# Kernel optimization log

Hardware: AMD Instinct MI355X
Metric: run time of the kernel (lower is better)

Reference implementation:

```python
import jax, jax.numpy as jnp
import numpy as np


def conv2d(x, w, b, pad=0):
    y = jax.lax.conv_general_dilated(x, w, (1, 1), [(pad, pad), (pad, pad)],
                                     dimension_numbers=('NCHW', 'OIHW', 'NCHW'))
    return y + b[None, :, None, None]


def leaky(x):
    return jnp.where(x >= 0, x, 0.1 * x)


def adaptive_pool3(x):
    # exact AdaptiveAvgPool2d((3,3)) when H,W divisible by 3
    B, C, H, W = x.shape
    return x.reshape(B, C, 3, H // 3, 3, W // 3).mean(axis=(3, 5))


def psf2otf(ker, H, W):
    # circularly shift PSF so its centre is at (0,0), then FFT (DWDN convention)
    B, C, kh, kw = ker.shape
    c = kh // 2 + 1
    psf = jnp.zeros((B, C, H, W), ker.dtype)
    psf = psf.at[:, :, :c, :c].set(ker[:, :, c - 1:, c - 1:])
    psf = psf.at[:, :, :c, -(c - 1):].set(ker[:, :, c - 1:, :c - 1])
    psf = psf.at[:, :, -(c - 1):, :c].set(ker[:, :, :c - 1, c - 1:])
    psf = psf.at[:, :, -(c - 1):, -(c - 1):].set(ker[:, :, :c - 1, :c - 1])
    return jnp.fft.fft2(psf)


def setup_inputs() -> dict:
    key = jax.random.key(0)
    ks = jax.random.split(key, 16)
    B, NF, C, H = 8, 64, 16, 246
    x = jax.random.normal(ks[0], (B, NF, H, H), jnp.float32)
    kernel = jax.random.uniform(ks[1], (B, 1, 21, 21), jnp.float32)
    kernel = kernel / kernel.sum(axis=(2, 3), keepdims=True)  # normalized blur PSF
    def w(k, shape):
        fan_in = shape[1] * shape[2] * shape[3]
        return jax.random.normal(k, shape, jnp.float32) / np.sqrt(fan_in)
    return {
        'x': x, 'kernel': kernel,
        'w_red': w(ks[2], (C, NF, 1, 1)), 'b_red': jnp.zeros((C,), jnp.float32),
        'w_g1': w(ks[3], (C, C, 3, 3)), 'b_g1': jnp.zeros((C,), jnp.float32),
        'w_g2': w(ks[4], (C, C, 3, 3)), 'b_g2': jnp.zeros((C,), jnp.float32),
        'w_g3': w(ks[5], (C, C, 3, 3)), 'b_g3': jnp.zeros((C,), jnp.float32),
        'w_g4': w(ks[6], (C, C, 1, 1)), 'b_g4': jnp.zeros((C,), jnp.float32),
        'w_exp': w(ks[7], (NF, C, 1, 1)), 'b_exp': jnp.zeros((NF,), jnp.float32),
    }


def reference(x, kernel, w_red, b_red, w_g1, b_g1, w_g2, b_g2, w_g3, b_g3,
              w_g4, b_g4, w_exp, b_exp):
    cls_feats = conv2d(x, w_red, b_red)                      # [B,C,H,W]
    h = leaky(conv2d(cls_feats, w_g1, b_g1))                 # valid 3x3 convs
    h = leaky(conv2d(h, w_g2, b_g2))
    h = conv2d(h, w_g3, b_g3)
    h = adaptive_pool3(h)                                    # [B,C,3,3]
    kernel_P = jnp.exp(conv2d(h, w_g4, b_g4))
    kernel_P = kernel_P - kernel_P.mean(axis=(2, 3), keepdims=True)

    ks_ = kernel.shape[-1]
    fp = jnp.pad(cls_feats, ((0, 0), (0, 0), (ks_, ks_), (ks_, ks_)), mode='edge')
    Hp, Wp = fp.shape[2], fp.shape[3]
    # batched Wiener deconvolution over all channels at once (replaces per-channel loop)
    Kf = psf2otf(kernel, Hp, Wp)                             # [B,1,Hp,Wp] complex
    Pf = psf2otf(kernel_P, Hp, Wp)                           # [B,C,Hp,Wp] complex
    denom = Kf.real ** 2 + Kf.imag ** 2 + Pf.real ** 2 + Pf.imag ** 2
    inv_ker = jnp.conj(Kf) / denom                           # conj(K)/(|K|^2+|P|^2)
    deblur = jnp.fft.ifft2(inv_ker * jnp.fft.fft2(fp)).real
    clear = deblur[:, :, ks_:-ks_, ks_:-ks_]
    return conv2d(clear, w_exp, b_exp)
```

## Files before the change

kernel.cpp:

```cpp
#include <hip/hip_runtime.h>
#include <hip/hip_bf16.h>

__device__ inline float2 cadd(float2 a, float2 b){ return make_float2(a.x+b.x, a.y+b.y); }
__device__ inline float2 csub(float2 a, float2 b){ return make_float2(a.x-b.x, a.y-b.y); }
__device__ inline float2 cmul(float2 a, float2 b){
    return make_float2(fmaf(a.x,b.x,-a.y*b.y), fmaf(a.x,b.y,a.y*b.x));
}

#define NPIX 60516
#define NFFT 288
#define NFFT2 82944
#define XW 152
#define SPLANE (NFFT*XW)

__device__ inline int lidx(int i, int c){ return i*8 + (i>>2) + c; }
#define LDSN 2376

template<bool INV>
__device__ inline void bf4(float2 a0, float2 a1, float2 a2, float2 a3,
                           float2& b0, float2& b1, float2& b2, float2& b3) {
    float2 t0=cadd(a0,a2), t1=csub(a0,a2), t2=cadd(a1,a3), t3=csub(a1,a3);
    b0=cadd(t0,t2); b2=csub(t0,t2);
    if (!INV) { b1=make_float2(t1.x+t3.y, t1.y-t3.x); b3=make_float2(t1.x-t3.y, t1.y+t3.x); }
    else      { b1=make_float2(t1.x-t3.y, t1.y+t3.x); b3=make_float2(t1.x+t3.y, t1.y-t3.x); }
}
template<bool INV>
__device__ inline void bf3(float2 a0, float2 a1, float2 a2,
                           float2& b0, float2& b1, float2& b2) {
    const float d = INV ? 0.8660254037844386f : -0.8660254037844386f;
    float2 tt=cadd(a1,a2), u=csub(a1,a2);
    b0=cadd(a0,tt);
    b1=make_float2(a0.x-0.5f*tt.x - d*u.y, a0.y-0.5f*tt.y + d*u.x);
    b2=make_float2(a0.x-0.5f*tt.x + d*u.y, a0.y-0.5f*tt.y - d*u.x);
}

template<bool INV>
__device__ inline void fft288_row(float2*& X, float2*& Y, int lane, const float2* __restrict__ tw) {
    auto TW = [&](int k) { float2 v = tw[k]; if (INV) v.y = -v.y; return v; };
    for (int p = lane; p < 72; p += 64) {
        float2 b0,b1,b2,b3;
        bf4<INV>(X[p], X[p+72], X[p+144], X[p+216], b0,b1,b2,b3);
        Y[4*p]=b0; Y[4*p+1]=cmul(b1,TW(p)); Y[4*p+2]=cmul(b2,TW(2*p)); Y[4*p+3]=cmul(b3,TW(3*p));
    }
    __syncthreads(); { float2* t=X; X=Y; Y=t; }
    for (int it = lane; it < 72; it += 64) {
        int p = it>>2, q = it&3, i0 = q+4*p;
        float2 b0,b1,b2,b3;
        bf4<INV>(X[i0], X[i0+72], X[i0+144], X[i0+216], b0,b1,b2,b3);
        int o = q+16*p;
        Y[o]=b0; Y[o+4]=cmul(b1,TW(4*p)); Y[o+8]=cmul(b2,TW(8*p)); Y[o+12]=cmul(b3,TW(12*p));
    }
    __syncthreads(); { float2* t=X; X=Y; Y=t; }
    for (int it = lane; it < 144; it += 64) {
        int p = it>>4, q = it&15, i0 = q+16*p;
        float2 a0=X[i0], a1=X[i0+144];
        int o = q+32*p;
        Y[o]=cadd(a0,a1); Y[o+16]=cmul(csub(a0,a1),TW(16*p));
    }
    __syncthreads(); { float2* t=X; X=Y; Y=t; }
    for (int it = lane; it < 96; it += 64) {
        int p = it>>5, q = it&31, i0 = q+32*p;
        float2 b0,b1,b2;
        bf3<INV>(X[i0], X[i0+96], X[i0+192], b0,b1,b2);
        int o = q+96*p;
        Y[o]=b0; Y[o+32]=cmul(b1,TW(32*p)); Y[o+64]=cmul(b2,TW(64*p));
    }
    __syncthreads(); { float2* t=X; X=Y; Y=t; }
    for (int q = lane; q < 96; q += 64) {
        float2 b0,b1,b2;
        bf3<INV>(X[q], X[q+96], X[q+192], b0,b1,b2);
        Y[q]=b0; Y[q+96]=b1; Y[q+192]=b2;
    }
    __syncthreads(); { float2* t=X; X=Y; Y=t; }
}

template<bool INV>
__device__ inline void fft288_s9(float2*& X, float2*& Y, int w, int c, const float2* __restrict__ tw) {
    auto TW = [&](int k) { float2 v = tw[k]; if (INV) v.y = -v.y; return v; };
    for (int p = w; p < 72; p += 32) {
        float2 b0,b1,b2,b3;
        bf4<INV>(X[lidx(p,c)], X[lidx(p+72,c)], X[lidx(p+144,c)], X[lidx(p+216,c)], b0,b1,b2,b3);
        Y[lidx(4*p,c)]=b0; Y[lidx(4*p+1,c)]=cmul(b1,TW(p));
        Y[lidx(4*p+2,c)]=cmul(b2,TW(2*p)); Y[lidx(4*p+3,c)]=cmul(b3,TW(3*p));
    }
    __syncthreads(); { float2* t=X; X=Y; Y=t; }
    for (int it = w; it < 72; it += 32) {
        int p = it>>2, q = it&3, i0 = q+4*p;
        float2 b0,b1,b2,b3;
        bf4<INV>(X[lidx(i0,c)], X[lidx(i0+72,c)], X[lidx(i0+144,c)], X[lidx(i0+216,c)], b0,b1,b2,b3);
        int o = q+16*p;
        Y[lidx(o,c)]=b0; Y[lidx(o+4,c)]=cmul(b1,TW(4*p));
        Y[lidx(o+8,c)]=cmul(b2,TW(8*p)); Y[lidx(o+12,c)]=cmul(b3,TW(12*p));
    }
    __syncthreads(); { float2* t=X; X=Y; Y=t; }
    for (int it = w; it < 144; it += 32) {
        int p = it>>4, q = it&15, i0 = q+16*p;
        float2 a0=X[lidx(i0,c)], a1=X[lidx(i0+144,c)];
        int o = q+32*p;
        Y[lidx(o,c)]=cadd(a0,a1); Y[lidx(o+16,c)]=cmul(csub(a0,a1),TW(16*p));
    }
    __syncthreads(); { float2* t=X; X=Y; Y=t; }
    for (int it = w; it < 96; it += 32) {
        int p = it>>5, q = it&31, i0 = q+32*p;
        float2 b0,b1,b2;
        bf3<INV>(X[lidx(i0,c)], X[lidx(i0+96,c)], X[lidx(i0+192,c)], b0,b1,b2);
        int o = q+96*p;
        Y[lidx(o,c)]=b0; Y[lidx(o+32,c)]=cmul(b1,TW(32*p)); Y[lidx(o+64,c)]=cmul(b2,TW(64*p));
    }
    __syncthreads(); { float2* t=X; X=Y; Y=t; }
    for (int q = w; q < 96; q += 32) {
        float2 b0,b1,b2;
        bf3<INV>(X[lidx(q,c)], X[lidx(q+96,c)], X[lidx(q+192,c)], b0,b1,b2);
        Y[lidx(q,c)]=b0; Y[lidx(q+96,c)]=b1; Y[lidx(q+192,c)]=b2;
    }
    __syncthreads(); { float2* t=X; X=Y; Y=t; }
}

__global__ void k_tw(float2* tw, float* pooled) {
    int t = threadIdx.x;
    if (t < NFFT) {
        double ang = -2.0 * 3.14159265358979323846 * (double)t / (double)NFFT;
        tw[t] = make_float2((float)cos(ang), (float)sin(ang));
    }
    for (int i = t; i < 1152; i += 320) pooled[i] = 0.f;
}

__global__ __launch_bounds__(256) void k_conv1x1_red(const float* __restrict__ x,
        const float* __restrict__ w, const float* __restrict__ bias, float* __restrict__ out) {
    int idx = blockIdx.x * 256 + threadIdx.x;
    if (idx >= 8 * NPIX) return;
    int b = idx / NPIX, p = idx % NPIX;
    const float* xb = x + (size_t)b * 64 * NPIX + p;
    float acc[16];
    #pragma unroll
    for (int co = 0; co < 16; co++) acc[co] = bias[co];
    for (int ci = 0; ci < 64; ci++) {
        float v = xb[(size_t)ci * NPIX];
        #pragma unroll
        for (int co = 0; co < 16; co++) acc[co] = fmaf(w[co*64+ci], v, acc[co]);
    }
    float* ob = out + (size_t)b * 16 * NPIX + p;
    #pragma unroll
    for (int co = 0; co < 16; co++) ob[(size_t)co*NPIX] = acc[co];
}

template<int HIN, bool LEAKY>
__global__ __launch_bounds__(256) void k_conv3x3(const float* __restrict__ in,
        const float* __restrict__ w, const float* __restrict__ bias, float* __restrict__ out) {
    const int HOUT = HIN - 2;
    const int GX = (HOUT + 3) / 4;
    int idx = blockIdx.x * 256 + threadIdx.x;
    if (idx >= 8 * HOUT * GX) return;
    int b  = idx / (HOUT * GX);
    int r  = idx % (HOUT * GX);
    int oy = r / GX;
    int ox0 = (r % GX) * 4;

    float acc[16][4];
    #pragma unroll
    for (int co = 0; co < 16; co++) {
        float bb = bias[co];
        #pragma unroll
        for (int px = 0; px < 4; px++) acc[co][px] = bb;
    }
    const float* ib = in + (size_t)b * 16 * HIN * HIN + (size_t)oy * HIN;
    for (int ci = 0; ci < 16; ci++) {
        const float* ic = ib + (size_t)ci * HIN * HIN;
        #pragma unroll
        for (int ky = 0; ky < 3; ky++) {
            float in6[6];
            #pragma unroll
            for (int j = 0; j < 6; j++) {
                int xx = ox0 + j;
                if (HOUT % 4 != 0) { if (xx > HIN - 1) xx = HIN - 1; }
                in6[j] = ic[ky * HIN + xx];
            }
            #pragma unroll
            for (int kx = 0; kx < 3; kx++) {
                #pragma unroll
                for (int co = 0; co < 16; co++) {
                    float wv = w[co*144 + ci*9 + ky*3 + kx];
                    #pragma unroll
                    for (int px = 0; px < 4; px++)
                        acc[co][px] = fmaf(wv, in6[px + kx], acc[co][px]);
                }
            }
        }
    }
    float* ob = out + (size_t)b * 16 * HOUT * HOUT + (size_t)oy * HOUT + ox0;
    #pragma unroll
    for (int co = 0; co < 16; co++) {
        #pragma unroll
        for (int px = 0; px < 4; px++) {
            if (HOUT % 4 == 0 || ox0 + px < HOUT) {
                float v = acc[co][px];
                if (LEAKY) v = (v >= 0.f) ? v : 0.1f * v;
                ob[(size_t)co * HOUT * HOUT + px] = v;
            }
        }
    }
}

__global__ __launch_bounds__(256) void k_conv3x3_pool(const float* __restrict__ in,
        const float* __restrict__ w, const float* __restrict__ bias, float* __restrict__ pooled) {
    const int HIN = 242, GX = 60;
    __shared__ float cs[144];
    int t = threadIdx.x;
    int b = blockIdx.x / 57;
    int r = (blockIdx.x % 57) * 256 + t;
    bool valid = r < 14400;
    float partial[16];
    int cell = 0;
    if (valid) {
        int oy = r / GX, ox0 = (r % GX) * 4;
        cell = (oy / 80) * 3 + (ox0 / 80);
        float acc[16][4];
        #pragma unroll
        for (int co = 0; co < 16; co++) {
            float bb = bias[co];
            #pragma unroll
            for (int px = 0; px < 4; px++) acc[co][px] = bb;
        }
        const float* ib = in + (size_t)b * 16 * HIN * HIN + (size_t)oy * HIN;
        for (int ci = 0; ci < 16; ci++) {
            const float* ic = ib + (size_t)ci * HIN * HIN;
            #pragma unroll
            for (int ky = 0; ky < 3; ky++) {
                float in6[6];
                #pragma unroll
                for (int j = 0; j < 6; j++) in6[j] = ic[ky * HIN + ox0 + j];
                #pragma unroll
                for (int kx = 0; kx < 3; kx++) {
                    #pragma unroll
                    for (int co = 0; co < 16; co++) {
                        float wv = w[co*144 + ci*9 + ky*3 + kx];
                        #pragma unroll
                        for (int px = 0; px < 4; px++)
                            acc[co][px] = fmaf(wv, in6[px + kx], acc[co][px]);
                    }
                }
            }
        }
        #pragma unroll
        for (int co = 0; co < 16; co++)
            partial[co] = (acc[co][0] + acc[co][1]) + (acc[co][2] + acc[co][3]);
    }
    if (t < 144) cs[t] = 0.f;
    __syncthreads();
    if (valid) {
        #pragma unroll
        for (int co = 0; co < 16; co++) atomicAdd(&cs[co*9 + cell], partial[co]);
    }
    __syncthreads();
    if (t < 144) atomicAdd(&pooled[b*144 + t], cs[t]);
}

__global__ void k_kernelP(const float* __restrict__ pooled, const float* __restrict__ w,
                          const float* __restrict__ bias, float* __restrict__ out) {
    int b = blockIdx.x / 16, co = blockIdx.x % 16;
    __shared__ float vals[9];
    int t = threadIdx.x;
    if (t < 9) {
        float a = 0.f;
        for (int ci = 0; ci < 16; ci++) a += pooled[(b*16+ci)*9 + t] * w[co*16+ci];
        vals[t] = expf(bias[co] + a * (1.f/6400.f));
    }
    __syncthreads();
    if (t < 9) {
        float m = 0.f;
        #pragma unroll
        for (int i = 0; i < 9; i++) m += vals[i];
        m *= (1.f/9.f);
        out[(b*16+co)*9 + t] = vals[t] - m;
    }
}

__global__ __launch_bounds__(256) void k_psfKT(const float* __restrict__ ker, float2* __restrict__ KfT) {
    int idx = blockIdx.x*256 + threadIdx.x;
    if (idx >= 8*NFFT2) return;
    int pos = idx % NFFT2, b = idx / NFFT2;
    int u = pos / NFFT, v = pos % NFFT;
    int ry = (v < 11) ? v+10 : ((v >= 278) ? v-278 : -1);
    int rx = (u < 11) ? u+10 : ((u >= 278) ? u-278 : -1);
    float val = (ry >= 0 && rx >= 0) ? ker[b*441 + ry*21 + rx] : 0.f;
    KfT[idx] = make_float2(val, 0.f);
}

template<bool INV>
__global__ __launch_bounds__(256) void k_fft_rows(float2* __restrict__ M, const float2* __restrict__ tw) {
    __shared__ float2 A[4][NFFT];
    __shared__ float2 B[4][NFFT];
    int t = threadIdx.x, w = t >> 6, lane = t & 63;
    size_t row = (size_t)blockIdx.x*4 + w;
    float2* X = A[w]; float2* Y = B[w];
    float2* s = M + row*NFFT;
    for (int j = lane; j < NFFT; j += 64) X[j] = s[j];
    __syncthreads();
    fft288_row<INV>(X, Y, lane, tw);
    for (int j = lane; j < NFFT; j += 64) s[j] = X[j];
}

template<bool INV>
__global__ __launch_bounds__(256) void k_fft_cols(float2* __restrict__ M, const float2* __restrict__ tw) {
    __shared__ float2 Abuf[LDSN];
    __shared__ float2 Bbuf[LDSN];
    int t = threadIdx.x, c = t & 7, w = t >> 3;
    int ch = blockIdx.x / 36, cg = blockIdx.x % 36;
    float2* base = M + (size_t)ch * NFFT2 + cg*8 + c;
    float2* X = Abuf; float2* Y = Bbuf;
    for (int r = w; r < NFFT; r += 32) X[lidx(r,c)] = base[(size_t)r * NFFT];
    __syncthreads();
    fft288_s9<INV>(X, Y, w, c, tw);
    for (int r = w; r < NFFT; r += 32) base[(size_t)r * NFFT] = X[lidx(r,c)];
}

__global__ __launch_bounds__(256) void k_fft_rows_pad_half(const float* __restrict__ cls,
        float2* __restrict__ S, const float2* __restrict__ tw) {
    __shared__ float2 A[4][NFFT];
    __shared__ float2 B[4][NFFT];
    int t = threadIdx.x, w = t >> 6, lane = t & 63;
    size_t row = (size_t)blockIdx.x*4 + w;
    int pc = (int)(row / NFFT), y = (int)(row % NFFT);
    int iy = min(max(y-21, 0), 245);
    const float* c0 = cls + (size_t)(2*pc)*NPIX + (size_t)iy*246;
    float2* X = A[w]; float2* Y = B[w];
    for (int j = lane; j < NFFT; j += 64) {
        int ix = min(max(j-21, 0), 245);
        X[j] = make_float2(c0[ix], c0[NPIX+ix]);
    }
    __syncthreads();
    fft288_row<false>(X, Y, lane, tw);
    int chA = (pc >> 3)*16 + (pc & 7)*2;
    float2* sA = S + (size_t)chA * SPLANE + (size_t)y * XW;
    float2* sB = sA + SPLANE;
    for (int x = lane; x < XW; x += 64) {
        float2 Av = make_float2(0.f, 0.f), Bv = make_float2(0.f, 0.f);
        if (x <= 144) {
            int m = (NFFT - x) % NFFT;
            float2 zk = X[x], zm = X[m];
            Av = make_float2(0.5f*(zk.x+zm.x),  0.5f*(zk.y-zm.y));
            Bv = make_float2(0.5f*(zk.y+zm.y), -0.5f*(zk.x-zm.x));
        }
        sA[x] = Av; sB[x] = Bv;
    }
}

__global__ __launch_bounds__(256) void k_fft_cols_filter(float2* __restrict__ S,
        const float2* __restrict__ KfT, const float* __restrict__ kP, const float2* __restrict__ tw) {
    __shared__ float2 Abuf[LDSN];
    __shared__ float2 Bbuf[LDSN];
    int t = threadIdx.x, c = t & 7, w = t >> 3;
    int g = blockIdx.x / 128, ch = blockIdx.x % 128;
    int xg = g*8 + c;
    int b = ch >> 4;
    float2* sb = S + (size_t)ch * SPLANE + xg;
    float2* X = Abuf; float2* Y = Bbuf;
    for (int r = w; r < NFFT; r += 32) X[lidx(r,c)] = sb[(size_t)r * XW];
    __syncthreads();
    fft288_s9<false>(X, Y, w, c, tw);
    {
        const float* p9 = kP + ch*9;
        float2 wx = tw[xg];
        const float2* Kcol = KfT + (size_t)b*NFFT2 + (size_t)xg*NFFT;
        for (int y = w; y < NFFT; y += 32) {
            float2 v = X[lidx(y,c)];
            float2 K = Kcol[y];
            float2 wy = tw[y];
            float2 R0 = make_float2(p9[1] + (p9[0]+p9[2])*wx.x, (p9[2]-p9[0])*wx.y);
            float2 R1 = make_float2(p9[4] + (p9[3]+p9[5])*wx.x, (p9[5]-p9[3])*wx.y);
            float2 R2 = make_float2(p9[7] + (p9[6]+p9[8])*wx.x, (p9[8]-p9[6])*wx.y);
            float2 P;
            P.x = R1.x + wy.x*(R0.x+R2.x) - wy.y*(R2.y-R0.y);
            P.y = R1.y + wy.x*(R0.y+R2.y) + wy.y*(R2.x-R0.x);
            float kk = K.x*K.x + K.y*K.y;
            float rcp = 1.0f / (kk + P.x*P.x + P.y*P.y);
            float2 H = make_float2(K.x*rcp, -K.y*rcp);
            Y[lidx(y,c)] = cmul(H, v);
        }
    }
    __syncthreads();
    { float2* tp = X; X = Y; Y = tp; }
    fft288_s9<true>(X, Y, w, c, tw);
    for (int r = w; r < NFFT; r += 32)
        if (r >= 21 && r < 267) sb[(size_t)r * XW] = X[lidx(r,c)];
}

__global__ __launch_bounds__(256) void k_ifft_rows_conv(const float2* __restrict__ S,
        const float* __restrict__ w_exp, const float* __restrict__ b_exp,
        float* __restrict__ out, const float2* __restrict__ tw) {
    __shared__ float2 Abuf[LDSN];
    __shared__ float2 Bbuf[LDSN];
    int t = threadIdx.x, c = t & 7, w = t >> 3;
    int b = blockIdx.x / 246;
    int rseq = blockIdx.x % 246;
    int y = rseq + 21;
    int chA = b*16 + 2*c;
    const float2* sA = S + (size_t)chA * SPLANE + (size_t)y * XW;
    const float2* sB = sA + SPLANE;
    float2* X = Abuf; float2* Y = Bbuf;
    for (int j = w; j < NFFT; j += 32) {
        float2 z;
        if (j <= 144) {
            float2 a = sA[j], bb = sB[j];
            z = make_float2(a.x - bb.y, a.y + bb.x);
        } else {
            int m = NFFT - j;
            float2 a = sA[m], bb = sB[m];
            z = make_float2(a.x + bb.y, bb.x - a.y);
        }
        X[lidx(j,c)] = z;
    }
    __syncthreads();
    fft288_s9<true>(X, Y, w, c, tw);
    if (t < 246) {
        const float sc = 1.0f / 82944.0f;
        float v[16];
        #pragma unroll
        for (int h = 0; h < 8; h++) {
            float2 z = X[lidx(t + 21, h)];
            v[2*h]   = z.x * sc;
            v[2*h+1] = z.y * sc;
        }
        float* ob = out + (size_t)b * 64 * NPIX + (size_t)rseq * 246 + t;
        #pragma unroll
        for (int co = 0; co < 64; co++) {
            float a = b_exp[co];
            #pragma unroll
            for (int ci = 0; ci < 16; ci++) a = fmaf(w_exp[co*16+ci], v[ci], a);
            ob[(size_t)co * NPIX] = a;
        }
    }
}

extern "C" void kernel_launch(void* const* d_in, const int* in_sizes, int n_in,
                              void* d_out, int out_size, void* d_ws, size_t ws_size,
                              hipStream_t stream) {
    const float* x     = (const float*)d_in[0];
    const float* ker   = (const float*)d_in[1];
    const float* w_red = (const float*)d_in[2];
    const float* b_red = (const float*)d_in[3];
    const float* w_g1  = (const float*)d_in[4];
    const float* b_g1  = (const float*)d_in[5];
    const float* w_g2  = (const float*)d_in[6];
    const float* b_g2  = (const float*)d_in[7];
    const float* w_g3  = (const float*)d_in[8];
    const float* b_g3  = (const float*)d_in[9];
    const float* w_g4  = (const float*)d_in[10];
    const float* b_g4  = (const float*)d_in[11];
    const float* w_exp = (const float*)d_in[12];
    const float* b_exp = (const float*)d_in[13];
    float* out = (float*)d_out;

    char* ws = (char*)d_ws;
    size_t off = 0;
    auto alloc = [&](size_t bytes) -> char* {
        char* p = ws + off; off += (bytes + 255) & ~(size_t)255; return p;
    };
    float*  cls    = (float*) alloc(7746048ull * 4);
    float2* S      = (float2*)alloc((size_t)128 * SPLANE * 8);
    float*  hb     = (float*) alloc(7495712ull * 4);
    float2* KfT    = (float2*)alloc((size_t)8 * NFFT2 * 8);
    float*  pooled = (float*) alloc(1152 * 4);
    float*  kP     = (float*) alloc(1152 * 4);
    float2* tw     = (float2*)alloc(288 * 8);
    float*  ha     = (float*)S;

    k_tw<<<1, 320, 0, stream>>>(tw, pooled);
    k_conv1x1_red<<<1892, 256, 0, stream>>>(x, w_red, b_red, cls);
    k_conv3x3<246, true ><<<466, 256, 0, stream>>>(cls, w_g1, b_g1, ha);
    k_conv3x3<244, true ><<<462, 256, 0, stream>>>(ha,  w_g2, b_g2, hb);
    k_conv3x3_pool<<<456, 256, 0, stream>>>(hb, w_g3, b_g3, pooled);
    k_kernelP<<<128, 64, 0, stream>>>(pooled, w_g4, b_g4, kP);

    k_psfKT<<<2592, 256, 0, stream>>>(ker, KfT);
    k_fft_rows<false><<<576, 256, 0, stream>>>(KfT, tw);
    k_fft_cols<false><<<288, 256, 0, stream>>>(KfT, tw);

    k_fft_rows_pad_half<<<4608, 256, 0, stream>>>(cls, S, tw);

    k_fft_cols_filter<<<19*128, 256, 0, stream>>>(S, KfT, kP, tw);

    k_ifft_rows_conv<<<1968, 256, 0, stream>>>(S, w_exp, b_exp, out, tw);
}
```

Baseline: 342.6 us.

## Replace LDS-staged radix FFT with register 16x18 FFT and vectorize convs

The five-stage shared-memory FFT-288, which needed a barrier after each stage, is replaced by a register-resident 16x18 decomposition (radix-16 then radix-18) with one LDS transpose. Every FFT kernel is restructured around a single padded LDS buffer holding 8 transforms per block, with one 32-thread group per transform. Separately, the 1x1 reduction conv now handles float4 pixel groups per thread. The final expansion conv computes two pixels per thread and splits output channels across half-blocks. The goals are fewer barriers and LDS round trips, and wider memory accesses, at the cost of only 18 or 16 of every 32 lanes doing work during the FFT stages and higher register use.

```diff
diff --git a/kernel.cpp b/kernel.cpp
--- a/kernel.cpp
+++ b/kernel.cpp
@@ -12,9 +12,7 @@
 #define NFFT2 82944
 #define XW 152
 #define SPLANE (NFFT*XW)
-
-__device__ inline int lidx(int i, int c){ return i*8 + (i>>2) + c; }
-#define LDSN 2376
+#define CST 312
 
 template<bool INV>
 __device__ inline void bf4(float2 a0, float2 a1, float2 a2, float2 a3,
@@ -33,87 +31,95 @@
     b1=make_float2(a0.x-0.5f*tt.x - d*u.y, a0.y-0.5f*tt.y + d*u.x);
     b2=make_float2(a0.x-0.5f*tt.x + d*u.y, a0.y-0.5f*tt.y - d*u.x);
 }
-
 template<bool INV>
-__device__ inline void fft288_row(float2*& X, float2*& Y, int lane, const float2* __restrict__ tw) {
-    auto TW = [&](int k) { float2 v = tw[k]; if (INV) v.y = -v.y; return v; };
-    for (int p = lane; p < 72; p += 64) {
+__device__ inline float2 twc(float cc, float ss){ return make_float2(cc, INV ? -ss : ss); }
+
+template<bool INV>
+__device__ inline void fft16r(float2* u) {
+    const float C[10]  = {1.f, 0.9238795325112867f, 0.7071067811865476f, 0.3826834323650898f, 0.f,
+                          -0.3826834323650898f, -0.7071067811865476f, -0.9238795325112867f, -1.f, -0.9238795325112867f};
+    const float Sn[10] = {0.f, -0.3826834323650898f, -0.7071067811865476f, -0.9238795325112867f, -1.f,
+                          -0.9238795325112867f, -0.7071067811865476f, -0.3826834323650898f, 0.f, 0.3826834323650898f};
+    float2 v[16];
+    #pragma unroll
+    for (int p = 0; p < 4; p++) {
         float2 b0,b1,b2,b3;
-        bf4<INV>(X[p], X[p+72], X[p+144], X[p+216], b0,b1,b2,b3);
-        Y[4*p]=b0; Y[4*p+1]=cmul(b1,TW(p)); Y[4*p+2]=cmul(b2,TW(2*p)); Y[4*p+3]=cmul(b3,TW(3*p));
-    }
-    __syncthreads(); { float2* t=X; X=Y; Y=t; }
-    for (int it = lane; it < 72; it += 64) {
-        int p = it>>2, q = it&3, i0 = q+4*p;
+        bf4<INV>(u[p], u[p+4], u[p+8], u[p+12], b0,b1,b2,b3);
+        v[4*p]   = b0;
+        v[4*p+1] = cmul(b1, twc<INV>(C[p],   Sn[p]));
+        v[4*p+2] = cmul(b2, twc<INV>(C[2*p], Sn[2*p]));
+        v[4*p+3] = cmul(b3, twc<INV>(C[3*p], Sn[3*p]));
+    }
+    #pragma unroll
+    for (int q = 0; q < 4; q++) {
         float2 b0,b1,b2,b3;
-        bf4<INV>(X[i0], X[i0+72], X[i0+144], X[i0+216], b0,b1,b2,b3);
-        int o = q+16*p;
-        Y[o]=b0; Y[o+4]=cmul(b1,TW(4*p)); Y[o+8]=cmul(b2,TW(8*p)); Y[o+12]=cmul(b3,TW(12*p));
-    }
-    __syncthreads(); { float2* t=X; X=Y; Y=t; }
-    for (int it = lane; it < 144; it += 64) {
-        int p = it>>4, q = it&15, i0 = q+16*p;
-        float2 a0=X[i0], a1=X[i0+144];
-        int o = q+32*p;
-        Y[o]=cadd(a0,a1); Y[o+16]=cmul(csub(a0,a1),TW(16*p));
-    }
-    __syncthreads(); { float2* t=X; X=Y; Y=t; }
-    for (int it = lane; it < 96; it += 64) {
-        int p = it>>5, q = it&31, i0 = q+32*p;
+        bf4<INV>(v[q], v[q+4], v[q+8], v[q+12], b0,b1,b2,b3);
+        u[q] = b0; u[q+4] = b1; u[q+8] = b2; u[q+12] = b3;
+    }
+}
+
+template<bool INV>
+__device__ inline void fft18r(float2* g) {
+    const float C[9]  = {1.f, 0.9396926207859084f, 0.7660444431189780f, 0.5f, 0.1736481776669304f,
+                         -0.1736481776669303f, -0.5f, -0.7660444431189779f, -0.9396926207859083f};
+    const float Sn[9] = {0.f, -0.3420201433256687f, -0.6427876096865393f, -0.8660254037844386f, -0.9848077530122080f,
+                         -0.9848077530122080f, -0.8660254037844387f, -0.6427876096865395f, -0.3420201433256689f};
+    float2 h[18];
+    #pragma unroll
+    for (int p = 0; p < 9; p++) {
+        float2 a = g[p], b = g[p+9];
+        h[2*p]   = cadd(a,b);
+        h[2*p+1] = cmul(csub(a,b), twc<INV>(C[p], Sn[p]));
+    }
+    float2 e[18];
+    #pragma unroll
+    for (int p = 0; p < 3; p++) {
+        #pragma unroll
+        for (int q = 0; q < 2; q++) {
+            float2 b0,b1,b2;
+            bf3<INV>(h[q+2*p], h[q+2*p+6], h[q+2*p+12], b0,b1,b2);
+            e[q+2*(3*p)]   = b0;
+            e[q+2*(3*p+1)] = cmul(b1, twc<INV>(C[2*p], Sn[2*p]));
+            e[q+2*(3*p+2)] = cmul(b2, twc<INV>(C[4*p], Sn[4*p]));
+        }
+    }
+    #pragma unroll
+    for (int q = 0; q < 6; q++) {
         float2 b0,b1,b2;
-        bf3<INV>(X[i0], X[i0+96], X[i0+192], b0,b1,b2);
-        int o = q+96*p;
-        Y[o]=b0; Y[o+32]=cmul(b1,TW(32*p)); Y[o+64]=cmul(b2,TW(64*p));
-    }
-    __syncthreads(); { float2* t=X; X=Y; Y=t; }
-    for (int q = lane; q < 96; q += 64) {
-        float2 b0,b1,b2;
-        bf3<INV>(X[q], X[q+96], X[q+192], b0,b1,b2);
-        Y[q]=b0; Y[q+96]=b1; Y[q+192]=b2;
-    }
-    __syncthreads(); { float2* t=X; X=Y; Y=t; }
+        bf3<INV>(e[q], e[q+6], e[q+12], b0,b1,b2);
+        g[q] = b0; g[q+6] = b1; g[q+12] = b2;
+    }
 }
 
 template<bool INV>
-__device__ inline void fft288_s9(float2*& X, float2*& Y, int w, int c, const float2* __restrict__ tw) {
-    auto TW = [&](int k) { float2 v = tw[k]; if (INV) v.y = -v.y; return v; };
-    for (int p = w; p < 72; p += 32) {
-        float2 b0,b1,b2,b3;
-        bf4<INV>(X[lidx(p,c)], X[lidx(p+72,c)], X[lidx(p+144,c)], X[lidx(p+216,c)], b0,b1,b2,b3);
-        Y[lidx(4*p,c)]=b0; Y[lidx(4*p+1,c)]=cmul(b1,TW(p));
-        Y[lidx(4*p+2,c)]=cmul(b2,TW(2*p)); Y[lidx(4*p+3,c)]=cmul(b3,TW(3*p));
-    }
-    __syncthreads(); { float2* t=X; X=Y; Y=t; }
-    for (int it = w; it < 72; it += 32) {
-        int p = it>>2, q = it&3, i0 = q+4*p;
-        float2 b0,b1,b2,b3;
-        bf4<INV>(X[lidx(i0,c)], X[lidx(i0+72,c)], X[lidx(i0+144,c)], X[lidx(i0+216,c)], b0,b1,b2,b3);
-        int o = q+16*p;
-        Y[lidx(o,c)]=b0; Y[lidx(o+4,c)]=cmul(b1,TW(4*p));
-        Y[lidx(o+8,c)]=cmul(b2,TW(8*p)); Y[lidx(o+12,c)]=cmul(b3,TW(12*p));
-    }
-    __syncthreads(); { float2* t=X; X=Y; Y=t; }
-    for (int it = w; it < 144; it += 32) {
-        int p = it>>4, q = it&15, i0 = q+16*p;
-        float2 a0=X[lidx(i0,c)], a1=X[lidx(i0+144,c)];
-        int o = q+32*p;
-        Y[lidx(o,c)]=cadd(a0,a1); Y[lidx(o+16,c)]=cmul(csub(a0,a1),TW(16*p));
-    }
-    __syncthreads(); { float2* t=X; X=Y; Y=t; }
-    for (int it = w; it < 96; it += 32) {
-        int p = it>>5, q = it&31, i0 = q+32*p;
-        float2 b0,b1,b2;
-        bf3<INV>(X[lidx(i0,c)], X[lidx(i0+96,c)], X[lidx(i0+192,c)], b0,b1,b2);
-        int o = q+96*p;
-        Y[lidx(o,c)]=b0; Y[lidx(o+32,c)]=cmul(b1,TW(32*p)); Y[lidx(o+64,c)]=cmul(b2,TW(64*p));
-    }
-    __syncthreads(); { float2* t=X; X=Y; Y=t; }
-    for (int q = w; q < 96; q += 32) {
-        float2 b0,b1,b2;
-        bf3<INV>(X[lidx(q,c)], X[lidx(q+96,c)], X[lidx(q+192,c)], b0,b1,b2);
-        Y[lidx(q,c)]=b0; Y[lidx(q+96,c)]=b1; Y[lidx(q+192,c)]=b2;
-    }
-    __syncthreads(); { float2* t=X; X=Y; Y=t; }
+__device__ inline void fft288_reg(float2* base, int l, const float2* __restrict__ tw) {
+    float2 u[16];
+    if (l < 18) {
+        #pragma unroll
+        for (int n1 = 0; n1 < 16; n1++) u[n1] = base[18*n1 + l];
+    }
+    __syncthreads();
+    if (l < 18) {
+        fft16r<INV>(u);
+        #pragma unroll
+        for (int k1 = 0; k1 < 16; k1++) {
+            float2 w = tw[l*k1];
+            if (INV) w.y = -w.y;
+            base[17*l + k1] = cmul(u[k1], w);
+        }
+    }
+    __syncthreads();
+    float2 g[18];
+    if (l < 16) {
+        #pragma unroll
+        for (int n2 = 0; n2 < 18; n2++) g[n2] = base[17*n2 + l];
+    }
+    __syncthreads();
+    if (l < 16) {
+        fft18r<INV>(g);
+        #pragma unroll
+        for (int k2 = 0; k2 < 18; k2++) base[16*k2 + l] = g[k2];
+    }
 }
 
 __global__ void k_tw(float2* tw, float* pooled) {
@@ -127,21 +133,28 @@
 
 __global__ __launch_bounds__(256) void k_conv1x1_red(const float* __restrict__ x,
         const float* __restrict__ w, const float* __restrict__ bias, float* __restrict__ out) {
+    const int NP4 = NPIX/4;
     int idx = blockIdx.x * 256 + threadIdx.x;
-    if (idx >= 8 * NPIX) return;
-    int b = idx / NPIX, p = idx % NPIX;
-    const float* xb = x + (size_t)b * 64 * NPIX + p;
-    float acc[16];
-    #pragma unroll
-    for (int co = 0; co < 16; co++) acc[co] = bias[co];
+    if (idx >= 8 * NP4) return;
+    int b = idx / NP4, p4 = idx % NP4;
+    const float4* xb = (const float4*)(x + (size_t)b * 64 * NPIX) + p4;
+    float4 acc[16];
+    #pragma unroll
+    for (int co = 0; co < 16; co++) { float bb = bias[co]; acc[co] = make_float4(bb,bb,bb,bb); }
     for (int ci = 0; ci < 64; ci++) {
-        float v = xb[(size_t)ci * NPIX];
-        #pragma unroll
-        for (int co = 0; co < 16; co++) acc[co] = fmaf(w[co*64+ci], v, acc[co]);
-    }
-    float* ob = out + (size_t)b * 16 * NPIX + p;
-    #pragma unroll
-    for (int co = 0; co < 16; co++) ob[(size_t)co*NPIX] = acc[co];
+        float4 v = xb[(size_t)ci * NP4];
+        #pragma unroll
+        for (int co = 0; co < 16; co++) {
+            float wv = w[co*64+ci];
+            acc[co].x = fmaf(wv, v.x, acc[co].x);
+            acc[co].y = fmaf(wv, v.y, acc[co].y);
+            acc[co].z = fmaf(wv, v.z, acc[co].z);
+            acc[co].w = fmaf(wv, v.w, acc[co].w);
+        }
+    }
+    float4* ob = (float4*)(out + (size_t)b * 16 * NPIX) + p4;
+    #pragma unroll
+    for (int co = 0; co < 16; co++) ob[(size_t)co*NP4] = acc[co];
 }
 
 template<int HIN, bool LEAKY>
@@ -286,148 +299,162 @@
     KfT[idx] = make_float2(val, 0.f);
 }
 
-template<bool INV>
-__global__ __launch_bounds__(256) void k_fft_rows(float2* __restrict__ M, const float2* __restrict__ tw) {
-    __shared__ float2 A[4][NFFT];
-    __shared__ float2 B[4][NFFT];
-    int t = threadIdx.x, w = t >> 6, lane = t & 63;
-    size_t row = (size_t)blockIdx.x*4 + w;
-    float2* X = A[w]; float2* Y = B[w];
-    float2* s = M + row*NFFT;
-    for (int j = lane; j < NFFT; j += 64) X[j] = s[j];
-    __syncthreads();
-    fft288_row<INV>(X, Y, lane, tw);
-    for (int j = lane; j < NFFT; j += 64) s[j] = X[j];
-}
-
-template<bool INV>
-__global__ __launch_bounds__(256) void k_fft_cols(float2* __restrict__ M, const float2* __restrict__ tw) {
-    __shared__ float2 Abuf[LDSN];
-    __shared__ float2 Bbuf[LDSN];
-    int t = threadIdx.x, c = t & 7, w = t >> 3;
-    int ch = blockIdx.x / 36, cg = blockIdx.x % 36;
-    float2* base = M + (size_t)ch * NFFT2 + cg*8 + c;
-    float2* X = Abuf; float2* Y = Bbuf;
-    for (int r = w; r < NFFT; r += 32) X[lidx(r,c)] = base[(size_t)r * NFFT];
-    __syncthreads();
-    fft288_s9<INV>(X, Y, w, c, tw);
-    for (int r = w; r < NFFT; r += 32) base[(size_t)r * NFFT] = X[lidx(r,c)];
+__global__ __launch_bounds__(256) void k_fftK_rows(float2* __restrict__ M, const float2* __restrict__ tw) {
+    __shared__ float2 L[8*CST];
+    int t = threadIdx.x, c = t>>5, l = t&31;
+    float2* mb = M + (size_t)blockIdx.x * 8 * NFFT;
+    for (int idx = t; idx < 2304; idx += 256) L[(idx/288)*CST + idx%288] = mb[idx];
+    __syncthreads();
+    fft288_reg<false>(L + c*CST, l, tw);
+    __syncthreads();
+    for (int idx = t; idx < 2304; idx += 256) mb[idx] = L[(idx/288)*CST + idx%288];
+}
+
+__global__ __launch_bounds__(256) void k_fftK_cols(float2* __restrict__ M, const float2* __restrict__ tw) {
+    __shared__ float2 L[8*CST];
+    int t = threadIdx.x, c = t>>5, l = t&31;
+    int ch = blockIdx.x / 36, grp = blockIdx.x % 36;
+    float2* mb = M + (size_t)ch * NFFT2 + grp*8;
+    for (int idx = t; idx < 2304; idx += 256) {
+        int f = idx & 7, yy = idx >> 3;
+        L[f*CST + yy] = mb[(size_t)yy * NFFT + f];
+    }
+    __syncthreads();
+    fft288_reg<false>(L + c*CST, l, tw);
+    __syncthreads();
+    for (int idx = t; idx < 2304; idx += 256) {
+        int f = idx & 7, yy = idx >> 3;
+        mb[(size_t)yy * NFFT + f] = L[f*CST + yy];
+    }
 }
 
 __global__ __launch_bounds__(256) void k_fft_rows_pad_half(const float* __restrict__ cls,
         float2* __restrict__ S, const float2* __restrict__ tw) {
-    __shared__ float2 A[4][NFFT];
-    __shared__ float2 B[4][NFFT];
-    int t = threadIdx.x, w = t >> 6, lane = t & 63;
-    size_t row = (size_t)blockIdx.x*4 + w;
-    int pc = (int)(row / NFFT), y = (int)(row % NFFT);
-    int iy = min(max(y-21, 0), 245);
-    const float* c0 = cls + (size_t)(2*pc)*NPIX + (size_t)iy*246;
-    float2* X = A[w]; float2* Y = B[w];
-    for (int j = lane; j < NFFT; j += 64) {
-        int ix = min(max(j-21, 0), 245);
-        X[j] = make_float2(c0[ix], c0[NPIX+ix]);
-    }
-    __syncthreads();
-    fft288_row<false>(X, Y, lane, tw);
+    __shared__ float2 L[8*CST];
+    int t = threadIdx.x, c = t>>5, l = t&31;
+    int pc = blockIdx.x / 36;
+    int y0 = (blockIdx.x % 36) * 8;
+    const float* c0base = cls + (size_t)(2*pc)*NPIX;
+    for (int idx = t; idx < 2304; idx += 256) {
+        int f = idx / 288, j = idx % 288;
+        int iy = min(max(y0 + f - 21, 0), 245);
+        int ix = min(max(j - 21, 0), 245);
+        const float* p = c0base + iy*246 + ix;
+        L[f*CST + j] = make_float2(p[0], p[NPIX]);
+    }
+    __syncthreads();
+    fft288_reg<false>(L + c*CST, l, tw);
+    __syncthreads();
     int chA = (pc >> 3)*16 + (pc & 7)*2;
-    float2* sA = S + (size_t)chA * SPLANE + (size_t)y * XW;
-    float2* sB = sA + SPLANE;
-    for (int x = lane; x < XW; x += 64) {
-        float2 Av = make_float2(0.f, 0.f), Bv = make_float2(0.f, 0.f);
-        if (x <= 144) {
-            int m = (NFFT - x) % NFFT;
-            float2 zk = X[x], zm = X[m];
-            Av = make_float2(0.5f*(zk.x+zm.x),  0.5f*(zk.y-zm.y));
-            Bv = make_float2(0.5f*(zk.y+zm.y), -0.5f*(zk.x-zm.x));
-        }
-        sA[x] = Av; sB[x] = Bv;
+    float2* sA = S + (size_t)chA * SPLANE;
+    for (int idx = t; idx < 8*XW; idx += 256) {
+        int f = idx / XW, x = idx % XW;
+        int y = y0 + f;
+        float2 zk = L[f*CST + x];
+        float2 zm = L[f*CST + ((288 - x) % 288)];
+        float2 Av = make_float2(0.5f*(zk.x+zm.x),  0.5f*(zk.y-zm.y));
+        float2 Bv = make_float2(0.5f*(zk.y+zm.y), -0.5f*(zk.x-zm.x));
+        sA[(size_t)y*XW + x] = Av;
+        sA[SPLANE + (size_t)y*XW + x] = Bv;
     }
 }
 
 __global__ __launch_bounds__(256) void k_fft_cols_filter(float2* __restrict__ S,
         const float2* __restrict__ KfT, const float* __restrict__ kP, const float2* __restrict__ tw) {
-    __shared__ float2 Abuf[LDSN];
-    __shared__ float2 Bbuf[LDSN];
-    int t = threadIdx.x, c = t & 7, w = t >> 3;
-    int g = blockIdx.x / 128, ch = blockIdx.x % 128;
-    int xg = g*8 + c;
+    __shared__ float2 L[8*CST];
+    int t = threadIdx.x, c = t>>5, l = t&31;
+    int g = blockIdx.x >> 7;
+    int ch = blockIdx.x & 127;
     int b = ch >> 4;
-    float2* sb = S + (size_t)ch * SPLANE + xg;
-    float2* X = Abuf; float2* Y = Bbuf;
-    for (int r = w; r < NFFT; r += 32) X[lidx(r,c)] = sb[(size_t)r * XW];
-    __syncthreads();
-    fft288_s9<false>(X, Y, w, c, tw);
+    float2* sc = S + (size_t)ch * SPLANE + g*8;
+    for (int idx = t; idx < 2304; idx += 256) {
+        int f = idx & 7, y = idx >> 3;
+        L[f*CST + y] = sc[(size_t)y * XW + f];
+    }
+    __syncthreads();
+    fft288_reg<false>(L + c*CST, l, tw);
+    __syncthreads();
     {
         const float* p9 = kP + ch*9;
-        float2 wx = tw[xg];
-        const float2* Kcol = KfT + (size_t)b*NFFT2 + (size_t)xg*NFFT;
-        for (int y = w; y < NFFT; y += 32) {
-            float2 v = X[lidx(y,c)];
-            float2 K = Kcol[y];
-            float2 wy = tw[y];
-            float2 R0 = make_float2(p9[1] + (p9[0]+p9[2])*wx.x, (p9[2]-p9[0])*wx.y);
-            float2 R1 = make_float2(p9[4] + (p9[3]+p9[5])*wx.x, (p9[5]-p9[3])*wx.y);
-            float2 R2 = make_float2(p9[7] + (p9[6]+p9[8])*wx.x, (p9[8]-p9[6])*wx.y);
+        float pv[9];
+        #pragma unroll
+        for (int i = 0; i < 9; i++) pv[i] = p9[i];
+        for (int idx = t; idx < 2304; idx += 256) {
+            int f = idx / 288, ky = idx % 288;
+            int x = g*8 + f;
+            float2 wx = tw[x], wy = tw[ky];
+            float2 K = KfT[(size_t)b*NFFT2 + (size_t)x*NFFT + ky];
+            float2 R0 = make_float2(pv[1] + (pv[0]+pv[2])*wx.x, (pv[2]-pv[0])*wx.y);
+            float2 R1 = make_float2(pv[4] + (pv[3]+pv[5])*wx.x, (pv[5]-pv[3])*wx.y);
+            float2 R2 = make_float2(pv[7] + (pv[6]+pv[8])*wx.x, (pv[8]-pv[6])*wx.y);
             float2 P;
             P.x = R1.x + wy.x*(R0.x+R2.x) - wy.y*(R2.y-R0.y);
             P.y = R1.y + wy.x*(R0.y+R2.y) + wy.y*(R2.x-R0.x);
             float kk = K.x*K.x + K.y*K.y;
             float rcp = 1.0f / (kk + P.x*P.x + P.y*P.y);
             float2 H = make_float2(K.x*rcp, -K.y*rcp);
-            Y[lidx(y,c)] = cmul(H, v);
-        }
-    }
-    __syncthreads();
-    { float2* tp = X; X = Y; Y = tp; }
-    fft288_s9<true>(X, Y, w, c, tw);
-    for (int r = w; r < NFFT; r += 32)
-        if (r >= 21 && r < 267) sb[(size_t)r * XW] = X[lidx(r,c)];
+            L[f*CST + ky] = cmul(H, L[f*CST + ky]);
+        }
+    }
+    __syncthreads();
+    fft288_reg<true>(L + c*CST, l, tw);
+    __syncthreads();
+    for (int idx = t; idx < 8*246; idx += 256) {
+        int f = idx & 7, rr = idx >> 3;
+        sc[(size_t)(rr + 21) * XW + f] = L[f*CST + rr + 21];
+    }
 }
 
 __global__ __launch_bounds__(256) void k_ifft_rows_conv(const float2* __restrict__ S,
         const float* __restrict__ w_exp, const float* __restrict__ b_exp,
         float* __restrict__ out, const float2* __restrict__ tw) {
-    __shared__ float2 Abuf[LDSN];
-    __shared__ float2 Bbuf[LDSN];
-    int t = threadIdx.x, c = t & 7, w = t >> 3;
+    __shared__ float2 L[8*CST];
+    int t = threadIdx.x, c = t>>5, l = t&31;
     int b = blockIdx.x / 246;
     int rseq = blockIdx.x % 246;
     int y = rseq + 21;
-    int chA = b*16 + 2*c;
-    const float2* sA = S + (size_t)chA * SPLANE + (size_t)y * XW;
-    const float2* sB = sA + SPLANE;
-    float2* X = Abuf; float2* Y = Bbuf;
-    for (int j = w; j < NFFT; j += 32) {
+    const float2* sbase = S + (size_t)(b*16) * SPLANE + (size_t)y * XW;
+    for (int idx = t; idx < 2304; idx += 256) {
+        int h = idx & 7, j = idx >> 3;
+        const float2* sA = sbase + (size_t)(2*h) * SPLANE;
         float2 z;
         if (j <= 144) {
-            float2 a = sA[j], bb = sB[j];
+            float2 a = sA[j], bb = sA[SPLANE + j];
             z = make_float2(a.x - bb.y, a.y + bb.x);
         } else {
-            int m = NFFT - j;
-            float2 a = sA[m], bb = sB[m];
+            int m = 288 - j;
+            float2 a = sA[m], bb = sA[SPLANE + m];
             z = make_float2(a.x + bb.y, bb.x - a.y);
         }
-        X[lidx(j,c)] = z;
-    }
-    __syncthreads();
-    fft288_s9<true>(X, Y, w, c, tw);
-    if (t < 246) {
+        L[h*CST + j] = z;
+    }
+    __syncthreads();
+    fft288_reg<true>(L + c*CST, l, tw);
+    __syncthreads();
+    int tt = t & 127;
+    int co0 = (t >> 7) * 32;
+    if (tt < 123) {
+        int x0 = 2*tt;
         const float sc = 1.0f / 82944.0f;
-        float v[16];
+        float v0[16], v1[16];
         #pragma unroll
         for (int h = 0; h < 8; h++) {
-            float2 z = X[lidx(t + 21, h)];
-            v[2*h]   = z.x * sc;
-            v[2*h+1] = z.y * sc;
-        }
-        float* ob = out + (size_t)b * 64 * NPIX + (size_t)rseq * 246 + t;
-        #pragma unroll
-        for (int co = 0; co < 64; co++) {
-            float a = b_exp[co];
+            float2 z0 = L[h*CST + x0 + 21];
+            float2 z1 = L[h*CST + x0 + 22];
+            v0[2*h] = z0.x*sc; v0[2*h+1] = z0.y*sc;
+            v1[2*h] = z1.x*sc; v1[2*h+1] = z1.y*sc;
+        }
+        float* ob = out + (size_t)b * 64 * NPIX + (size_t)rseq * 246 + x0;
+        #pragma unroll
+        for (int co = 0; co < 32; co++) {
+            const float* wr = w_exp + (co0 + co)*16;
+            float a0 = b_exp[co0 + co], a1 = a0;
             #pragma unroll
-            for (int ci = 0; ci < 16; ci++) a = fmaf(w_exp[co*16+ci], v[ci], a);
-            ob[(size_t)co * NPIX] = a;
+            for (int ci = 0; ci < 16; ci++) {
+                a0 = fmaf(wr[ci], v0[ci], a0);
+                a1 = fmaf(wr[ci], v1[ci], a1);
+            }
+            *(float2*)(ob + (size_t)(co0 + co) * NPIX) = make_float2(a0, a1);
         }
     }
 }
@@ -466,17 +493,17 @@
     float*  ha     = (float*)S;
 
     k_tw<<<1, 320, 0, stream>>>(tw, pooled);
-    k_conv1x1_red<<<1892, 256, 0, stream>>>(x, w_red, b_red, cls);
+    k_conv1x1_red<<<473, 256, 0, stream>>>(x, w_red, b_red, cls);
     k_conv3x3<246, true ><<<466, 256, 0, stream>>>(cls, w_g1, b_g1, ha);
     k_conv3x3<244, true ><<<462, 256, 0, stream>>>(ha,  w_g2, b_g2, hb);
     k_conv3x3_pool<<<456, 256, 0, stream>>>(hb, w_g3, b_g3, pooled);
     k_kernelP<<<128, 64, 0, stream>>>(pooled, w_g4, b_g4, kP);
 
     k_psfKT<<<2592, 256, 0, stream>>>(ker, KfT);
-    k_fft_rows<false><<<576, 256, 0, stream>>>(KfT, tw);
-    k_fft_cols<false><<<288, 256, 0, stream>>>(KfT, tw);
-
-    k_fft_rows_pad_half<<<4608, 256, 0, stream>>>(cls, S, tw);
+    k_fftK_rows<<<288, 256, 0, stream>>>(KfT, tw);
+    k_fftK_cols<<<288, 256, 0, stream>>>(KfT, tw);
+
+    k_fft_rows_pad_half<<<2304, 256, 0, stream>>>(cls, S, tw);
 
     k_fft_cols_filter<<<19*128, 256, 0, stream>>>(S, KfT, kP, tw);
 
```

After: 378.4 us. 10.5% more time.
